# Kernel optimization log

Measured on AMD Instinct MI355X. Metric: run time of the kernel, lower is better.

Reference implementation:

```python
import jax, jax.numpy as jnp
import numpy as np

B, N, DIM, IN_DIM, H = 8, 3136, 147, 64, 1
HD = IN_DIM // H          # per-head value/key dim = 64
MLP_HID = int(IN_DIM * 1.0)
EPS = 1e-5


def _ln(x, w, b):
    m = jnp.mean(x, axis=-1, keepdims=True)
    v = jnp.mean((x - m) ** 2, axis=-1, keepdims=True)
    return (x - m) / jnp.sqrt(v + EPS) * w + b


def setup_inputs() -> dict:
    key = jax.random.key(0)
    ks = jax.random.split(key, 12)
    r = lambda k, shp, s=0.02: (jax.random.normal(k, shp, dtype=jnp.float32) * s)
    return {
        "x": jax.random.normal(ks[0], (B, N, DIM), dtype=jnp.float32),
        "norm1_w": jnp.ones((DIM,), jnp.float32),
        "norm1_b": jnp.zeros((DIM,), jnp.float32),
        "qkv_w": r(ks[1], (3 * IN_DIM, DIM)),
        "scale": jnp.full((H,), (DIM // H) ** -0.5, dtype=jnp.float32),
        "proj_w": r(ks[2], (IN_DIM, IN_DIM)),
        "proj_b": jnp.zeros((IN_DIM,), jnp.float32),
        "norm2_w": jnp.ones((IN_DIM,), jnp.float32),
        "norm2_b": jnp.zeros((IN_DIM,), jnp.float32),
        "fc1_w": r(ks[3], (MLP_HID, IN_DIM)),
        "fc1_b": jnp.zeros((MLP_HID,), jnp.float32),
        "fc2_w": r(ks[4], (IN_DIM, MLP_HID)),
        "fc2_b": jnp.zeros((IN_DIM,), jnp.float32),
    }


def reference(x, norm1_w, norm1_b, qkv_w, scale, proj_w, proj_b,
              norm2_w, norm2_b, fc1_w, fc1_b, fc2_w, fc2_b):
    h = _ln(x, norm1_w, norm1_b)                               # [B,N,DIM]
    qkv = jnp.einsum('bnc,oc->bno', h, qkv_w)                  # [B,N,3*IN_DIM]
    qkv = qkv.reshape(B, N, 3, H, HD).transpose(2, 0, 3, 1, 4)  # [3,B,H,N,HD]
    q, k, v = qkv[0], qkv[1], qkv[2]
    # LMSA: learnable per-head scale + diagonal (self) exclusion mask
    attn = jnp.einsum('bhid,bhjd->bhij', q, k) * scale[None, :, None, None]
    eye = jnp.eye(N, dtype=bool)
    attn = jnp.where(eye[None, None], -jnp.inf, attn)
    attn = jax.nn.softmax(attn, axis=-1)
    o = jnp.einsum('bhij,bhjd->bhid', attn, v)                 # [B,H,N,HD]
    o = o.transpose(0, 2, 1, 3).reshape(B, N, IN_DIM)
    o = jnp.einsum('bnd,od->bno', o, proj_w) + proj_b
    # num_heads == 1 -> residual is v itself
    x_attn = v[:, 0] + o                                       # [B,N,IN_DIM]
    h2 = _ln(x_attn, norm2_w, norm2_b)
    h2 = jax.nn.gelu(jnp.einsum('bnd,hd->bnh', h2, fc1_w) + fc1_b,
                     approximate=False)
    h2 = jnp.einsum('bnh,oh->bno', h2, fc2_w) + fc2_b
    return x_attn + h2
```

## Files before the change

### kernel.cpp

```cpp
#include <hip/hip_runtime.h>
#include <math.h>
#include <stdint.h>

#define B_    8
#define N_    3136
#define DIM_  147
#define KP_   160
#define TOK_  (B_*N_)
#define QKV3_ 192

typedef __attribute__((ext_vector_type(4))) float f32x4;
typedef __attribute__((ext_vector_type(4))) unsigned int u32x4;
typedef __attribute__((ext_vector_type(8))) short short8;
typedef union { short8 s; u32x4 u; } pk8;

static __device__ __forceinline__ unsigned short f2b(float f){
  unsigned int u = __float_as_uint(f);
  u += 0x7fffu + ((u>>16)&1u);
  return (unsigned short)(u>>16);
}
static __device__ __forceinline__ unsigned int pk2(float a, float b){
  return ((unsigned int)f2b(b)<<16) | (unsigned int)f2b(a);
}
static __device__ __forceinline__ unsigned int pk2t(float a, float b){
  return (__float_as_uint(b) & 0xffff0000u) | (__float_as_uint(a)>>16);
}
static __device__ __forceinline__ float b2f(unsigned short s){
  return __uint_as_float(((unsigned int)s)<<16);
}

#define GLD16(gp, lp) __builtin_amdgcn_global_load_lds( \
    reinterpret_cast<const uint32_t __attribute__((address_space(1)))*>(reinterpret_cast<uintptr_t>(gp)), \
    reinterpret_cast<uint32_t __attribute__((address_space(3)))*>(reinterpret_cast<uintptr_t>(lp)), \
    16, 0, 0)

__global__ __launch_bounds__(256) void k_prep(const float* __restrict__ qkvw,
                                              const float* __restrict__ projw,
                                              const float* __restrict__ fc1w,
                                              const float* __restrict__ fc2w,
                                              unsigned short* __restrict__ wp,
                                              unsigned short* __restrict__ wpj,
                                              unsigned short* __restrict__ w1b,
                                              unsigned short* __restrict__ w2b){
  int idx = blockIdx.x*256 + threadIdx.x;
  if(idx < QKV3_*KP_){
    int n = idx / KP_, k = idx - n*KP_;
    wp[idx] = f2b((k < DIM_) ? qkvw[n*DIM_ + k] : 0.f);
  }
  if(idx < 4096){
    wpj[idx] = f2b(projw[idx]);
    w1b[idx] = f2b(fc1w[idx]);
    w2b[idx] = f2b(fc2w[idx]);
  }
}

__global__ __launch_bounds__(256,2) void k_qkv(const float* __restrict__ x,
                                               const float* __restrict__ w1,
                                               const float* __restrict__ b1,
                                               const unsigned short* __restrict__ wp,
                                               const float* __restrict__ scale,
                                               unsigned short* __restrict__ qb,
                                               unsigned short* __restrict__ kb,
                                               unsigned short* __restrict__ vtb,
                                               unsigned short* __restrict__ vfb){
  __shared__ alignas(16) unsigned short A_[32*168];
  __shared__ alignas(16) unsigned short VT[64*36];
  int tid = threadIdx.x;
  int w = tid>>6, lane = tid&63, quad = lane>>4, l16 = lane&15;
  int t0 = blockIdx.x*32;
  float sc2 = scale[0] * 1.44269504089f;

  {
    int g = tid>>3, e = tid&7;
    const float* xr = x + (size_t)(t0+g)*147;
    float xv[19];
    float s = 0.f, sq = 0.f;
    #pragma unroll
    for(int i=0;i<19;i++){
      int col = e + 8*i;
      float v = (col < 147) ? xr[col] : 0.f;
      xv[i] = v; s += v; sq += v*v;
    }
    s  += __shfl_xor(s,1,64);  s  += __shfl_xor(s,2,64);  s  += __shfl_xor(s,4,64);
    sq += __shfl_xor(sq,1,64); sq += __shfl_xor(sq,2,64); sq += __shfl_xor(sq,4,64);
    float mean = s*(1.f/147.f);
    float var  = sq*(1.f/147.f) - mean*mean;
    float rstd = rsqrtf(var + 1e-5f);
    #pragma unroll
    for(int i=0;i<19;i++){
      int col = e + 8*i;
      if(col < 147) A_[g*168 + col] = f2b((xv[i]-mean)*rstd*w1[col] + b1[col]);
    }
    #pragma unroll
    for(int i=0;i<2;i++){
      int col = 144 + e + 8*i;
      if(col >= 147 && col < 160) A_[g*168 + col] = 0;
    }
  }
  __syncthreads();
  int mh = (w&1)*16, cb = (w>>1)*96;
  short8 Af[5];
  #pragma unroll
  for(int kk=0;kk<5;kk++)
    Af[kk] = *(const short8*)(A_ + (mh+l16)*168 + kk*32 + quad*8);
  f32x4 acc[6];
  #pragma unroll
  for(int i=0;i<6;i++) acc[i] = (f32x4){0.f,0.f,0.f,0.f};
  #pragma unroll
  for(int nt=0;nt<6;nt++){
    #pragma unroll
    for(int kk=0;kk<5;kk++){
      short8 Bf = *(const short8*)(wp + (size_t)(cb+nt*16+l16)*160 + kk*32 + quad*8);
      acc[nt] = __builtin_amdgcn_mfma_f32_16x16x32_bf16(Af[kk], Bf, acc[nt], 0,0,0);
    }
  }
  #pragma unroll
  for(int nt=0;nt<6;nt++){
    int o = cb + nt*16 + l16;
    #pragma unroll
    for(int r=0;r<4;r++){
      int tl = mh + quad*4 + r;
      int mg = t0 + tl;
      float val = acc[nt][r];
      if(o < 64){
        qb[(size_t)mg*64 + o] = f2b(val*sc2);
      } else if(o < 128){
        kb[(size_t)mg*64 + (o-64)] = f2b(val);
      } else {
        int hd = o - 128;
        unsigned short vb = f2b(val);
        vfb[(size_t)mg*64 + hd] = vb;
        VT[hd*36 + tl] = vb;
      }
    }
  }
  __syncthreads();
  {
    int b = t0 / N_, n0 = t0 - b*N_;
    const unsigned int* VT32 = (const unsigned int*)VT;
    unsigned int* vg = (unsigned int*)vtb + ((size_t)b*64)*(N_/2) + (n0>>1);
    for(int rep=0;rep<4;rep++){
      int f = rep*256 + tid;
      int row = f>>4, c = f&15;
      vg[(size_t)row*(N_/2) + c] = VT32[row*18 + c];
    }
  }
}

__global__ __launch_bounds__(128,4) void k_attn(const unsigned short* __restrict__ qb,
                                                const unsigned short* __restrict__ kb,
                                                const unsigned short* __restrict__ vtb,
                                                unsigned short* __restrict__ Opart,
                                                float* __restrict__ lpart){
  __shared__ alignas(16) unsigned int L[4096];
  unsigned int* Ks = L;
  unsigned int* Vs = L + 2048;
  int tid = threadIdx.x;
  int w = tid>>6, lane = tid&63, quad = lane>>4, l16 = lane&15;
  int qt = blockIdx.x, sp = blockIdx.y, b = blockIdx.z;
  int kv0 = (sp*49)>>2, kv1 = ((sp+1)*49)>>2;

  short8 Qf[2][2];
  {
    const unsigned short* qg = qb + ((size_t)b*N_ + qt*64 + w*32)*64;
    #pragma unroll
    for(int qs=0;qs<2;qs++)
      #pragma unroll
      for(int kk=0;kk<2;kk++)
        Qf[qs][kk] = *(const short8*)(qg + (qs*16+l16)*64 + kk*32 + quad*8);
  }
  int koffL[4], voffL[4];
  {
    int pl = lane>>3, cl = lane&7;
    #pragma unroll
    for(int rr=0;rr<4;rr++){
      int p = w*32 + rr*8 + pl;
      int sig = (p&32)|((p&12)<<1)|((p&16)>>2)|(p&3);
      int cx = cl ^ (p&7);
      koffL[rr] = sig*128 + cx*16;
      voffL[rr] = p*(N_*2) + cx*16;
    }
  }
  const char* kBase = (const char*)kb + (size_t)b*N_*128;
  const char* vBase = (const char*)vtb + (size_t)b*64*(size_t)(N_*2);

  f32x4 O[2][4];
  #pragma unroll
  for(int qs=0;qs<2;qs++) for(int j=0;j<4;j++) O[qs][j] = (f32x4){0.f,0.f,0.f,0.f};
  float lr[2] = {0.f, 0.f};
  const unsigned short* Ksh = (const unsigned short*)Ks;
  const unsigned short* Vsh = (const unsigned short*)Vs;
  int r7 = l16&7;
  int ku0 = (quad ^ r7)*8;
  int ku1 = ((4+quad) ^ r7)*8;
  int dloc = w*32 + l16;

  for(int kvt=kv0; kvt<kv1; ++kvt){
    __syncthreads();
    {
      const char* kT = kBase + (size_t)kvt*8192;
      const char* vT = vBase + (size_t)kvt*128;
      #pragma unroll
      for(int rr=0;rr<4;rr++){
        GLD16(kT + koffL[rr], (char*)Ks + (w*32+rr*8)*128);
        GLD16(vT + voffL[rr], (char*)Vs + (w*32+rr*8)*128);
      }
    }
    __syncthreads();

    pk8 Pb[2][2];
    #pragma unroll
    for(int qs=0;qs<2;qs++){
      f32x4 S[4];
      #pragma unroll
      for(int jt=0;jt<4;jt++){
        short8 Kf0 = *(const short8*)(Ksh + jt*1024 + l16*64 + ku0);
        short8 Kf1 = *(const short8*)(Ksh + jt*1024 + l16*64 + ku1);
        f32x4 z = (f32x4){0.f,0.f,0.f,0.f};
        S[jt] = __builtin_amdgcn_mfma_f32_16x16x32_bf16(Kf0, Qf[qs][0], z, 0,0,0);
        S[jt] = __builtin_amdgcn_mfma_f32_16x16x32_bf16(Kf1, Qf[qs][1], S[jt], 0,0,0);
      }
      float p[4][4];
      if(kvt == qt){
        int dl = dloc + qs*16;
        #pragma unroll
        for(int jt=0;jt<4;jt++){
          int kvb = (jt>>1)*32 + (jt&1)*4 + quad*8;
          #pragma unroll
          for(int r=0;r<4;r++){
            float pv = (kvb + r == dl) ? 0.f : __builtin_amdgcn_exp2f(S[jt][r]);
            p[jt][r] = pv; lr[qs] += pv;
          }
        }
      } else {
        #pragma unroll
        for(int jt=0;jt<4;jt++)
          #pragma unroll
          for(int r=0;r<4;r++){
            float pv = __builtin_amdgcn_exp2f(S[jt][r]);
            p[jt][r] = pv; lr[qs] += pv;
          }
      }
      Pb[qs][0].u = (u32x4){ pk2t(p[0][0],p[0][1]), pk2t(p[0][2],p[0][3]),
                             pk2t(p[1][0],p[1][1]), pk2t(p[1][2],p[1][3]) };
      Pb[qs][1].u = (u32x4){ pk2t(p[2][0],p[2][1]), pk2t(p[2][2],p[2][3]),
                             pk2t(p[3][0],p[3][1]), pk2t(p[3][2],p[3][3]) };
    }
    #pragma unroll
    for(int jt2=0;jt2<4;jt2++){
      short8 Vf0 = *(const short8*)(Vsh + jt2*1024 + l16*64 + ku0);
      short8 Vf1 = *(const short8*)(Vsh + jt2*1024 + l16*64 + ku1);
      O[0][jt2] = __builtin_amdgcn_mfma_f32_16x16x32_bf16(Vf0, Pb[0][0].s, O[0][jt2], 0,0,0);
      O[0][jt2] = __builtin_amdgcn_mfma_f32_16x16x32_bf16(Vf1, Pb[0][1].s, O[0][jt2], 0,0,0);
      O[1][jt2] = __builtin_amdgcn_mfma_f32_16x16x32_bf16(Vf0, Pb[1][0].s, O[1][jt2], 0,0,0);
      O[1][jt2] = __builtin_amdgcn_mfma_f32_16x16x32_bf16(Vf1, Pb[1][1].s, O[1][jt2], 0,0,0);
    }
  }
  lr[0] += __shfl_xor(lr[0],16,64); lr[0] += __shfl_xor(lr[0],32,64);
  lr[1] += __shfl_xor(lr[1],16,64); lr[1] += __shfl_xor(lr[1],32,64);
  __syncthreads();
  #pragma unroll
  for(int qs=0;qs<2;qs++){
    int q = w*32 + qs*16 + l16;
    #pragma unroll
    for(int jt2=0;jt2<4;jt2++){
      L[q*36 + jt2*8 + quad*2]     = pk2(O[qs][jt2][0], O[qs][jt2][1]);
      L[q*36 + jt2*8 + quad*2 + 1] = pk2(O[qs][jt2][2], O[qs][jt2][3]);
    }
  }
  if(quad == 0){
    size_t lbase = (size_t)sp*TOK_ + (size_t)b*N_ + qt*64 + w*32;
    lpart[lbase + l16]      = lr[0];
    lpart[lbase + 16 + l16] = lr[1];
  }
  __syncthreads();
  {
    unsigned int* og = (unsigned int*)(Opart + ((size_t)sp*TOK_ + (size_t)b*N_ + qt*64)*64);
    for(int rep=0;rep<4;rep++){
      int f = rep*128 + tid;
      int row = f>>3, c = f&7;
      *(u32x4*)(og + row*32 + c*4) = *(const u32x4*)&L[row*36 + c*4];
    }
  }
}

__global__ __launch_bounds__(128) void k_mlp(const unsigned short* __restrict__ Opart,
                                             const float* __restrict__ lpart,
                                             const unsigned short* __restrict__ vfb,
                                             const unsigned short* __restrict__ wpj,
                                             const unsigned short* __restrict__ w1b,
                                             const unsigned short* __restrict__ w2b,
                                             const float* __restrict__ projb,
                                             const float* __restrict__ n2w,
                                             const float* __restrict__ n2b,
                                             const float* __restrict__ fc1b,
                                             const float* __restrict__ fc2b,
                                             float* __restrict__ out){
  __shared__ alignas(16) unsigned short Xs[32*72];
  unsigned int* Xs32 = (unsigned int*)Xs;
  int tid = threadIdx.x;
  int w = tid>>6, lane = tid&63, quad = lane>>4, l16 = lane&15;
  int t0 = blockIdx.x*32;

  #pragma unroll
  for(int i=0;i<2;i++){
    int f = i*128 + tid;
    int row = f>>3, c = f&7;
    float lo[4] = {0,0,0,0}, hi[4] = {0,0,0,0};
    float lsum = 0.f;
    #pragma unroll
    for(int s=0;s<4;s++){
      u32x4 a = *((const u32x4*)(Opart + ((size_t)s*TOK_ + t0)*64) + row*8 + c);
      #pragma unroll
      for(int k=0;k<4;k++){
        lo[k] += __uint_as_float(a[k]<<16);
        hi[k] += __uint_as_float(a[k] & 0xffff0000u);
      }
      lsum += lpart[(size_t)s*TOK_ + t0 + row];
    }
    float linv = 1.f/lsum;
    u32x4 o;
    #pragma unroll
    for(int k=0;k<4;k++) o[k] = pk2(lo[k]*linv, hi[k]*linv);
    *(u32x4*)&Xs32[row*36 + c*4] = o;
  }
  __syncthreads();

  short8 Af[2];
  #pragma unroll
  for(int kk=0;kk<2;kk++)
    Af[kk] = *(const short8*)(Xs + (w*16+l16)*72 + kk*32 + quad*8);
  f32x4 acc[4];
  #pragma unroll
  for(int i=0;i<4;i++) acc[i] = (f32x4){0.f,0.f,0.f,0.f};
  #pragma unroll
  for(int jt=0;jt<4;jt++)
    #pragma unroll
    for(int kk=0;kk<2;kk++){
      short8 Bf = *(const short8*)(wpj + (jt*16+l16)*64 + kk*32 + quad*8);
      acc[jt] = __builtin_amdgcn_mfma_f32_16x16x32_bf16(Af[kk], Bf, acc[jt], 0,0,0);
    }
  float xa[4][4];
  #pragma unroll
  for(int jt=0;jt<4;jt++){
    int col = jt*16 + l16;
    float pb = projb[col];
    #pragma unroll
    for(int r=0;r<4;r++){
      int tg = t0 + w*16 + quad*4 + r;
      xa[jt][r] = acc[jt][r] + pb + b2f(vfb[(size_t)tg*64 + col]);
    }
  }
  #pragma unroll
  for(int r=0;r<4;r++){
    float s = 0.f, sq = 0.f;
    #pragma unroll
    for(int jt=0;jt<4;jt++){ s += xa[jt][r]; sq += xa[jt][r]*xa[jt][r]; }
    s  += __shfl_xor(s,1,64);  s  += __shfl_xor(s,2,64);
    s  += __shfl_xor(s,4,64);  s  += __shfl_xor(s,8,64);
    sq += __shfl_xor(sq,1,64); sq += __shfl_xor(sq,2,64);
    sq += __shfl_xor(sq,4,64); sq += __shfl_xor(sq,8,64);
    float mu = s*(1.f/64.f);
    float var = sq*(1.f/64.f) - mu*mu;
    float rstd = rsqrtf(var + 1e-5f);
    #pragma unroll
    for(int jt=0;jt<4;jt++){
      int col = jt*16 + l16;
      Xs[(w*16+quad*4+r)*72 + col] = f2b((xa[jt][r]-mu)*rstd*n2w[col] + n2b[col]);
    }
  }
  #pragma unroll
  for(int kk=0;kk<2;kk++)
    Af[kk] = *(const short8*)(Xs + (w*16+l16)*72 + kk*32 + quad*8);
  f32x4 acc2[4];
  #pragma unroll
  for(int i=0;i<4;i++) acc2[i] = (f32x4){0.f,0.f,0.f,0.f};
  #pragma unroll
  for(int jt=0;jt<4;jt++)
    #pragma unroll
    for(int kk=0;kk<2;kk++){
      short8 Bf = *(const short8*)(w1b + (jt*16+l16)*64 + kk*32 + quad*8);
      acc2[jt] = __builtin_amdgcn_mfma_f32_16x16x32_bf16(Af[kk], Bf, acc2[jt], 0,0,0);
    }
  #pragma unroll
  for(int jt=0;jt<4;jt++){
    int col = jt*16 + l16;
    float fb = fc1b[col];
    #pragma unroll
    for(int r=0;r<4;r++){
      float g = acc2[jt][r] + fb;
      float z = g*0.70710678118f;
      float az = fabsf(z);
      float t = 1.f/(1.f + 0.3275911f*az);
      float poly = ((((1.061405429f*t - 1.453152027f)*t + 1.421413741f)*t - 0.284496736f)*t + 0.254829592f)*t;
      float er = 1.f - poly*__builtin_amdgcn_exp2f(-az*az*1.44269504089f);
      er = (z < 0.f) ? -er : er;
      Xs[(w*16+quad*4+r)*72 + col] = f2b(0.5f*g*(1.f + er));
    }
  }
  #pragma unroll
  for(int kk=0;kk<2;kk++)
    Af[kk] = *(const short8*)(Xs + (w*16+l16)*72 + kk*32 + quad*8);
  f32x4 acc3[4];
  #pragma unroll
  for(int i=0;i<4;i++) acc3[i] = (f32x4){0.f,0.f,0.f,0.f};
  #pragma unroll
  for(int jt=0;jt<4;jt++)
    #pragma unroll
    for(int kk=0;kk<2;kk++){
      short8 Bf = *(const short8*)(w2b + (jt*16+l16)*64 + kk*32 + quad*8);
      acc3[jt] = __builtin_amdgcn_mfma_f32_16x16x32_bf16(Af[kk], Bf, acc3[jt], 0,0,0);
    }
  #pragma unroll
  for(int jt=0;jt<4;jt++){
    int col = jt*16 + l16;
    float ob2 = fc2b[col];
    #pragma unroll
    for(int r=0;r<4;r++){
      int tg = t0 + w*16 + quad*4 + r;
      out[(size_t)tg*64 + col] = xa[jt][r] + acc3[jt][r] + ob2;
    }
  }
}

extern "C" void kernel_launch(void* const* d_in, const int* in_sizes, int n_in,
                              void* d_out, int out_size, void* d_ws, size_t ws_size,
                              hipStream_t stream){
  const float* x     = (const float*)d_in[0];
  const float* n1w   = (const float*)d_in[1];
  const float* n1b   = (const float*)d_in[2];
  const float* qkvw  = (const float*)d_in[3];
  const float* scale = (const float*)d_in[4];
  const float* projw = (const float*)d_in[5];
  const float* projb = (const float*)d_in[6];
  const float* n2w   = (const float*)d_in[7];
  const float* n2b   = (const float*)d_in[8];
  const float* fc1w  = (const float*)d_in[9];
  const float* fc1b  = (const float*)d_in[10];
  const float* fc2w  = (const float*)d_in[11];
  const float* fc2b  = (const float*)d_in[12];

  char* base = (char*)d_ws;
  unsigned short* wp  = (unsigned short*)(base + 0);
  unsigned short* wpj = (unsigned short*)(base + 61440);
  unsigned short* w1b = (unsigned short*)(base + 69632);
  unsigned short* w2b = (unsigned short*)(base + 77824);
  unsigned short* qb  = (unsigned short*)(base + 86016);
  unsigned short* kb  = (unsigned short*)(base + 3297280);
  unsigned short* vtb = (unsigned short*)(base + 6508544);
  unsigned short* vfb = (unsigned short*)(base + 9719808);
  unsigned short* Op  = (unsigned short*)(base + 12931072);
  float*          lp  = (float*)(base + 25776128);

  hipLaunchKernelGGL(k_prep, dim3(120),      dim3(256), 0, stream,
                     qkvw, projw, fc1w, fc2w, wp, wpj, w1b, w2b);
  hipLaunchKernelGGL(k_qkv,  dim3(TOK_/32),  dim3(256), 0, stream,
                     x, n1w, n1b, wp, scale, qb, kb, vtb, vfb);
  hipLaunchKernelGGL(k_attn, dim3(49,4,8),   dim3(128), 0, stream, qb, kb, vtb, Op, lp);
  hipLaunchKernelGGL(k_mlp,  dim3(TOK_/32),  dim3(128), 0, stream, Op, lp, vfb,
                     wpj, w1b, w2b, projb, n2w, n2b, fc1b, fc2b, (float*)d_out);
}
```

Baseline: 154.2 us.

## Load attention K/V fragments directly to registers with double-buffered prefetch

```diff
diff --git a/kernel.cpp b/kernel.cpp
--- a/kernel.cpp
+++ b/kernel.cpp
@@ -28,11 +28,6 @@
 static __device__ __forceinline__ float b2f(unsigned short s){
   return __uint_as_float(((unsigned int)s)<<16);
 }
-
-#define GLD16(gp, lp) __builtin_amdgcn_global_load_lds( \
-    reinterpret_cast<const uint32_t __attribute__((address_space(1)))*>(reinterpret_cast<uintptr_t>(gp)), \
-    reinterpret_cast<uint32_t __attribute__((address_space(3)))*>(reinterpret_cast<uintptr_t>(lp)), \
-    16, 0, 0)
 
 __global__ __launch_bounds__(256) void k_prep(const float* __restrict__ qkvw,
                                               const float* __restrict__ projw,
@@ -147,82 +142,71 @@
   }
 }
 
-__global__ __launch_bounds__(128,4) void k_attn(const unsigned short* __restrict__ qb,
-                                                const unsigned short* __restrict__ kb,
-                                                const unsigned short* __restrict__ vtb,
-                                                unsigned short* __restrict__ Opart,
-                                                float* __restrict__ lpart){
-  __shared__ alignas(16) unsigned int L[4096];
-  unsigned int* Ks = L;
-  unsigned int* Vs = L + 2048;
-  int tid = threadIdx.x;
-  int w = tid>>6, lane = tid&63, quad = lane>>4, l16 = lane&15;
-  int qt = blockIdx.x, sp = blockIdx.y, b = blockIdx.z;
+__global__ __launch_bounds__(64,2) void k_attn(const unsigned short* __restrict__ qb,
+                                               const unsigned short* __restrict__ kb,
+                                               const unsigned short* __restrict__ vtb,
+                                               unsigned short* __restrict__ Opart,
+                                               float* __restrict__ lpart){
+  __shared__ alignas(16) unsigned int L[32*36];
+  int lane = threadIdx.x & 63;
+  int quad = lane>>4, l16 = lane&15;
+  int qw = blockIdx.x, sp = blockIdx.y, b = blockIdx.z;
+  int q0 = qw*32;
+  int qt = qw>>1;
   int kv0 = (sp*49)>>2, kv1 = ((sp+1)*49)>>2;
 
   short8 Qf[2][2];
   {
-    const unsigned short* qg = qb + ((size_t)b*N_ + qt*64 + w*32)*64;
+    const unsigned short* qg = qb + ((size_t)b*N_ + q0)*64;
     #pragma unroll
     for(int qs=0;qs<2;qs++)
       #pragma unroll
       for(int kk=0;kk<2;kk++)
         Qf[qs][kk] = *(const short8*)(qg + (qs*16+l16)*64 + kk*32 + quad*8);
   }
-  int koffL[4], voffL[4];
-  {
-    int pl = lane>>3, cl = lane&7;
-    #pragma unroll
-    for(int rr=0;rr<4;rr++){
-      int p = w*32 + rr*8 + pl;
-      int sig = (p&32)|((p&12)<<1)|((p&16)>>2)|(p&3);
-      int cx = cl ^ (p&7);
-      koffL[rr] = sig*128 + cx*16;
-      voffL[rr] = p*(N_*2) + cx*16;
-    }
-  }
-  const char* kBase = (const char*)kb + (size_t)b*N_*128;
-  const char* vBase = (const char*)vtb + (size_t)b*64*(size_t)(N_*2);
+  int koff[4], voff[4];
+  #pragma unroll
+  for(int jt=0;jt<4;jt++){
+    int p = jt*16 + l16;
+    int sig = (p&32)|((p&12)<<1)|((p&16)>>2)|(p&3);
+    koff[jt] = sig*128 + quad*16;
+    voff[jt] = ((jt*16 + l16)*N_ + quad*8)*2;
+  }
+  const char* kT = (const char*)kb + (size_t)b*N_*128 + (size_t)kv0*8192;
+  const char* vT = (const char*)vtb + (size_t)b*64*(size_t)(N_*2) + (size_t)kv0*128;
 
   f32x4 O[2][4];
   #pragma unroll
   for(int qs=0;qs<2;qs++) for(int j=0;j<4;j++) O[qs][j] = (f32x4){0.f,0.f,0.f,0.f};
   float lr[2] = {0.f, 0.f};
-  const unsigned short* Ksh = (const unsigned short*)Ks;
-  const unsigned short* Vsh = (const unsigned short*)Vs;
-  int r7 = l16&7;
-  int ku0 = (quad ^ r7)*8;
-  int ku1 = ((4+quad) ^ r7)*8;
-  int dloc = w*32 + l16;
-
-  for(int kvt=kv0; kvt<kv1; ++kvt){
-    __syncthreads();
-    {
-      const char* kT = kBase + (size_t)kvt*8192;
-      const char* vT = vBase + (size_t)kvt*128;
-      #pragma unroll
-      for(int rr=0;rr<4;rr++){
-        GLD16(kT + koffL[rr], (char*)Ks + (w*32+rr*8)*128);
-        GLD16(vT + voffL[rr], (char*)Vs + (w*32+rr*8)*128);
-      }
-    }
-    __syncthreads();
-
-    pk8 Pb[2][2];
+
+  auto loadK = [&](short8* Kf, const char* base){
+    #pragma unroll
+    for(int jt=0;jt<4;jt++){
+      Kf[jt*2]   = *(const short8*)(base + koff[jt]);
+      Kf[jt*2+1] = *(const short8*)(base + koff[jt] + 64);
+    }
+  };
+  auto loadV = [&](short8* Vf, const char* base){
+    #pragma unroll
+    for(int j=0;j<4;j++){
+      Vf[j*2]   = *(const short8*)(base + voff[j]);
+      Vf[j*2+1] = *(const short8*)(base + voff[j] + 64);
+    }
+  };
+  auto tile = [&](const short8* Kf, const short8* Vf, int kvt){
     #pragma unroll
     for(int qs=0;qs<2;qs++){
       f32x4 S[4];
       #pragma unroll
       for(int jt=0;jt<4;jt++){
-        short8 Kf0 = *(const short8*)(Ksh + jt*1024 + l16*64 + ku0);
-        short8 Kf1 = *(const short8*)(Ksh + jt*1024 + l16*64 + ku1);
         f32x4 z = (f32x4){0.f,0.f,0.f,0.f};
-        S[jt] = __builtin_amdgcn_mfma_f32_16x16x32_bf16(Kf0, Qf[qs][0], z, 0,0,0);
-        S[jt] = __builtin_amdgcn_mfma_f32_16x16x32_bf16(Kf1, Qf[qs][1], S[jt], 0,0,0);
+        S[jt] = __builtin_amdgcn_mfma_f32_16x16x32_bf16(Kf[jt*2],   Qf[qs][0], z, 0,0,0);
+        S[jt] = __builtin_amdgcn_mfma_f32_16x16x32_bf16(Kf[jt*2+1], Qf[qs][1], S[jt], 0,0,0);
       }
       float p[4][4];
       if(kvt == qt){
-        int dl = dloc + qs*16;
+        int dl = q0 + qs*16 + l16 - kvt*64;
         #pragma unroll
         for(int jt=0;jt<4;jt++){
           int kvb = (jt>>1)*32 + (jt&1)*4 + quad*8;
@@ -241,27 +225,38 @@
             p[jt][r] = pv; lr[qs] += pv;
           }
       }
-      Pb[qs][0].u = (u32x4){ pk2t(p[0][0],p[0][1]), pk2t(p[0][2],p[0][3]),
-                             pk2t(p[1][0],p[1][1]), pk2t(p[1][2],p[1][3]) };
-      Pb[qs][1].u = (u32x4){ pk2t(p[2][0],p[2][1]), pk2t(p[2][2],p[2][3]),
-                             pk2t(p[3][0],p[3][1]), pk2t(p[3][2],p[3][3]) };
-    }
-    #pragma unroll
-    for(int jt2=0;jt2<4;jt2++){
-      short8 Vf0 = *(const short8*)(Vsh + jt2*1024 + l16*64 + ku0);
-      short8 Vf1 = *(const short8*)(Vsh + jt2*1024 + l16*64 + ku1);
-      O[0][jt2] = __builtin_amdgcn_mfma_f32_16x16x32_bf16(Vf0, Pb[0][0].s, O[0][jt2], 0,0,0);
-      O[0][jt2] = __builtin_amdgcn_mfma_f32_16x16x32_bf16(Vf1, Pb[0][1].s, O[0][jt2], 0,0,0);
-      O[1][jt2] = __builtin_amdgcn_mfma_f32_16x16x32_bf16(Vf0, Pb[1][0].s, O[1][jt2], 0,0,0);
-      O[1][jt2] = __builtin_amdgcn_mfma_f32_16x16x32_bf16(Vf1, Pb[1][1].s, O[1][jt2], 0,0,0);
-    }
-  }
+      pk8 Pb0, Pb1;
+      Pb0.u = (u32x4){ pk2t(p[0][0],p[0][1]), pk2t(p[0][2],p[0][3]),
+                       pk2t(p[1][0],p[1][1]), pk2t(p[1][2],p[1][3]) };
+      Pb1.u = (u32x4){ pk2t(p[2][0],p[2][1]), pk2t(p[2][2],p[2][3]),
+                       pk2t(p[3][0],p[3][1]), pk2t(p[3][2],p[3][3]) };
+      #pragma unroll
+      for(int jt2=0;jt2<4;jt2++){
+        O[qs][jt2] = __builtin_amdgcn_mfma_f32_16x16x32_bf16(Vf[jt2*2],   Pb0.s, O[qs][jt2], 0,0,0);
+        O[qs][jt2] = __builtin_amdgcn_mfma_f32_16x16x32_bf16(Vf[jt2*2+1], Pb1.s, O[qs][jt2], 0,0,0);
+      }
+    }
+  };
+
+  short8 K0[8], K1[8], V0[8], V1[8];
+  loadK(K0, kT); loadV(V0, vT);
+  int t = kv0;
+  while(true){
+    loadK(K1, kT + 8192); loadV(V1, vT + 128);
+    tile(K0, V0, t);
+    ++t; kT += 8192; vT += 128;
+    if(t == kv1) break;
+    loadK(K0, kT + 8192); loadV(V0, vT + 128);
+    tile(K1, V1, t);
+    ++t; kT += 8192; vT += 128;
+    if(t == kv1) break;
+  }
+
   lr[0] += __shfl_xor(lr[0],16,64); lr[0] += __shfl_xor(lr[0],32,64);
   lr[1] += __shfl_xor(lr[1],16,64); lr[1] += __shfl_xor(lr[1],32,64);
-  __syncthreads();
   #pragma unroll
   for(int qs=0;qs<2;qs++){
-    int q = w*32 + qs*16 + l16;
+    int q = qs*16 + l16;
     #pragma unroll
     for(int jt2=0;jt2<4;jt2++){
       L[q*36 + jt2*8 + quad*2]     = pk2(O[qs][jt2][0], O[qs][jt2][1]);
@@ -269,15 +264,15 @@
     }
   }
   if(quad == 0){
-    size_t lbase = (size_t)sp*TOK_ + (size_t)b*N_ + qt*64 + w*32;
+    size_t lbase = (size_t)sp*TOK_ + (size_t)b*N_ + q0;
     lpart[lbase + l16]      = lr[0];
     lpart[lbase + 16 + l16] = lr[1];
   }
-  __syncthreads();
   {
-    unsigned int* og = (unsigned int*)(Opart + ((size_t)sp*TOK_ + (size_t)b*N_ + qt*64)*64);
+    unsigned int* og = (unsigned int*)(Opart + ((size_t)sp*TOK_ + (size_t)b*N_ + q0)*64);
+    #pragma unroll
     for(int rep=0;rep<4;rep++){
-      int f = rep*128 + tid;
+      int f = rep*64 + lane;
       int row = f>>3, c = f&7;
       *(u32x4*)(og + row*32 + c*4) = *(const u32x4*)&L[row*36 + c*4];
     }
@@ -456,7 +451,7 @@
                      qkvw, projw, fc1w, fc2w, wp, wpj, w1b, w2b);
   hipLaunchKernelGGL(k_qkv,  dim3(TOK_/32),  dim3(256), 0, stream,
                      x, n1w, n1b, wp, scale, qb, kb, vtb, vfb);
-  hipLaunchKernelGGL(k_attn, dim3(49,4,8),   dim3(128), 0, stream, qb, kb, vtb, Op, lp);
+  hipLaunchKernelGGL(k_attn, dim3(98,4,8),   dim3(64),  0, stream, qb, kb, vtb, Op, lp);
   hipLaunchKernelGGL(k_mlp,  dim3(TOK_/32),  dim3(128), 0, stream, Op, lp, vfb,
                      wpj, w1b, w2b, projb, n2w, n2b, fc1b, fc2b, (float*)d_out);
 }
```

Result: slower. 201.3 us (+30.6%).
